# Kernel optimization log

Hardware: AMD Instinct MI355X
Metric: run time of the kernel (lower is better)

The kernel has to match this reference:

```python
import jax, jax.numpy as jnp
import numpy as np
import math

B, S, H, NH = 4, 1024, 1024, 16
HD = H // NH  # 64
MAX_REL = 127


def relative_position_encoding(depth, max_length, max_relative_position):
    vocab_size = max_relative_position * 2 + 1
    range_vec = np.arange(max_length)
    distance = range_vec[None, :] - range_vec[:, None]  # matches range_mat - range_mat.T
    final_mat = np.clip(distance, -max_relative_position, max_relative_position) + max_relative_position
    position = np.arange(vocab_size, dtype=np.float32)[:, None]
    div_term = np.exp(np.arange(0, depth, 2, dtype=np.float32) * (-math.log(10000.0) / depth))
    table = np.zeros((vocab_size, depth), dtype=np.float32)
    table[:, 0::2] = np.sin(position * div_term)
    table[:, 1::2] = np.cos(position * div_term)
    return jnp.asarray(table[final_mat])  # [max_length, max_length, depth]


def setup_inputs() -> dict:
    key = jax.random.key(0)
    ks = jax.random.split(key, 4)
    sc = 0.02
    return {
        "hidden_states": jax.random.normal(ks[0], (B, S, H), dtype=jnp.float32),
        "Wq": jax.random.normal(ks[1], (H, H), dtype=jnp.float32) * sc,
        "bq": jnp.zeros((H,), dtype=jnp.float32),
        "Wk": jax.random.normal(ks[2], (H, H), dtype=jnp.float32) * sc,
        "bk": jnp.zeros((H,), dtype=jnp.float32),
        "Wv": jax.random.normal(ks[3], (H, H), dtype=jnp.float32) * sc,
        "bv": jnp.zeros((H,), dtype=jnp.float32),
        "rel_pos": relative_position_encoding(HD, S, MAX_REL),  # [S, S, HD] sinusoidal buffer
    }


def reference(hidden_states, Wq, bq, Wk, bk, Wv, bv, rel_pos):
    b, s, h = hidden_states.shape

    def heads(x):  # [b,s,h] -> [b,nh,s,hd]
        return x.reshape(b, s, NH, HD).transpose(0, 2, 1, 3)

    q = heads(hidden_states @ Wq.T + bq)
    k = heads(hidden_states @ Wk.T + bk)
    v = heads(hidden_states @ Wv.T + bv)

    scores = jnp.einsum("bhqd,bhkd->bhqk", q, k)
    # query-relative-key positional term
    scores = scores + jnp.einsum("bhqd,qkd->bhqk", q, rel_pos)
    scores = scores / math.sqrt(HD)

    probs = jax.nn.softmax(scores, axis=-1)  # dropout p=0 (eval)

    ctx = jnp.einsum("bhqk,bhkd->bhqd", probs, v)
    # prob-relative-value positional term
    ctx = ctx + jnp.einsum("bhqk,qkd->bhqd", probs, rel_pos)

    return ctx.transpose(0, 2, 1, 3).reshape(b, s, h)
```

## Files before the change

### kernel.cpp

```cpp
#include <hip/hip_runtime.h>
#include <stdint.h>


typedef __bf16 bf16x8 __attribute__((ext_vector_type(8)));
typedef float f32x4 __attribute__((ext_vector_type(4)));
typedef uint16_t u16x8 __attribute__((ext_vector_type(8)));
typedef uint16_t u16x4 __attribute__((ext_vector_type(4)));

#define K2E 0.18033688011112042f

__device__ __forceinline__ float hw_exp2(float x) {
    return __builtin_amdgcn_exp2f(x);
}
__device__ __forceinline__ uint16_t f2bf(float f) {
    uint32_t u = __builtin_bit_cast(uint32_t, f);
    return (uint16_t)((u + 0x7FFFu + ((u >> 16) & 1u)) >> 16);
}
__device__ __forceinline__ uint16_t f2bf_rn(float f) {
    return __builtin_bit_cast(uint16_t, (__bf16)f);
}
__device__ __forceinline__ float bf2f(uint16_t h) {
    uint32_t u = ((uint32_t)h) << 16;
    return __builtin_bit_cast(float, u);
}
__device__ __forceinline__ f32x4 mfma16(bf16x8 a, bf16x8 b, f32x4 c) {
    return __builtin_amdgcn_mfma_f32_16x16x32_bf16(a, b, c, 0, 0, 0);
}
__device__ __forceinline__ bf16x8 ldg8(const uint16_t* p) {
    return __builtin_bit_cast(bf16x8, *(const u16x8*)p);
}
__device__ __forceinline__ bf16x8 lds8(const void* base, int byteoff) {
    return __builtin_bit_cast(bf16x8, *(const u16x8*)((const char*)base + byteoff));
}

__global__ void k_cast_all(const float* __restrict__ hs, const float* __restrict__ wq,
                           const float* __restrict__ wk, const float* __restrict__ wv,
                           const float* __restrict__ rel,
                           uint16_t* __restrict__ hs_bf, uint16_t* __restrict__ w_bf,
                           uint16_t* __restrict__ tab, uint16_t* __restrict__ tabT) {
    int b = blockIdx.x;
    if (b >= 3584) {
        int idx = (b - 3584) * 256 + threadIdx.x;
        int j = idx >> 6, d = idx & 63;
        float v = 0.0f;
        if (j < 255) v = rel[((size_t)512 * 1024 + (512 + j - 127)) * 64 + d];
        uint16_t h = f2bf(v);
        tab[j * 64 + d] = h;
        tabT[d * 256 + j] = h;
        return;
    }
    const float* src;
    uint16_t* dst;
    int i;
    if (b < 2048)      { src = hs; dst = hs_bf;           i = b * 256 + threadIdx.x; }
    else if (b < 2560) { src = wq; dst = w_bf;            i = (b - 2048) * 256 + threadIdx.x; }
    else if (b < 3072) { src = wk; dst = w_bf + 1048576;  i = (b - 2560) * 256 + threadIdx.x; }
    else               { src = wv; dst = w_bf + 2097152;  i = (b - 3072) * 256 + threadIdx.x; }
    float4 a = ((const float4*)src)[2 * i];
    float4 c = ((const float4*)src)[2 * i + 1];
    u16x8 o;
    o[0] = f2bf(a.x); o[1] = f2bf(a.y); o[2] = f2bf(a.z); o[3] = f2bf(a.w);
    o[4] = f2bf(c.x); o[5] = f2bf(c.y); o[6] = f2bf(c.z); o[7] = f2bf(c.w);
    ((u16x8*)dst)[i] = o;
}

__launch_bounds__(256)
__global__ void k_gemm_qkv3(const uint16_t* __restrict__ A, const uint16_t* __restrict__ Wt,
                            const float* __restrict__ bq, const float* __restrict__ bk,
                            const float* __restrict__ bvp, uint16_t* __restrict__ qout,
                            uint16_t* __restrict__ kout, uint16_t* __restrict__ vt) {
    __shared__ uint16_t As[128 * 64];
    __shared__ uint16_t Bs[128 * 64];
    int bid = blockIdx.x;
    int xcd = bid & 7, idx = bid >> 3;
    int m0 = (xcd * 4 + (idx & 3)) * 128;
    int n0 = (idx >> 2) * 128;
    int tid = threadIdx.x;
    int w = tid >> 6, l = tid & 63, lg = l >> 4, ln = l & 15;
    int wm = w >> 1, wn = w & 1;
    int lrow = tid >> 3, lcol = (tid & 7) * 8;
    f32x4 acc[4][4] = {};
    for (int kt = 0; kt < 16; ++kt) {
        int k0 = kt * 64;
        __syncthreads();
#pragma unroll
        for (int c = 0; c < 4; ++c) {
            int row = c * 32 + lrow;
            __builtin_amdgcn_global_load_lds(
                (const __attribute__((address_space(1))) void*)(A + (size_t)(m0 + row) * 1024 + k0 + lcol),
                (__attribute__((address_space(3))) void*)&As[row * 64 + lcol], 16, 0, 0);
            __builtin_amdgcn_global_load_lds(
                (const __attribute__((address_space(1))) void*)(Wt + (size_t)(n0 + row) * 1024 + k0 + lcol),
                (__attribute__((address_space(3))) void*)&Bs[row * 64 + lcol], 16, 0, 0);
        }
        __syncthreads();
#pragma unroll
        for (int ks = 0; ks < 2; ++ks) {
            bf16x8 af[4], bfr[4];
#pragma unroll
            for (int mi = 0; mi < 4; ++mi)
                af[mi] = ldg8(&As[(wm * 64 + mi * 16 + ln) * 64 + ks * 32 + lg * 8]);
#pragma unroll
            for (int ni = 0; ni < 4; ++ni)
                bfr[ni] = ldg8(&Bs[(wn * 64 + ni * 16 + ln) * 64 + ks * 32 + lg * 8]);
#pragma unroll
            for (int mi = 0; mi < 4; ++mi)
#pragma unroll
                for (int ni = 0; ni < 4; ++ni)
                    acc[mi][ni] = mfma16(af[mi], bfr[ni], acc[mi][ni]);
        }
    }
    int b = m0 >> 10, srow = (m0 & 1023) + wm * 64;
#pragma unroll
    for (int ni = 0; ni < 4; ++ni) {
        int n = n0 + wn * 64 + ni * 16 + ln;
        int which = n >> 10, nr = n & 1023;
        const float* bp = which == 0 ? bq : (which == 1 ? bk : bvp);
        float bb = bp[nr];
        int h = nr >> 6, d = nr & 63;
        if (which < 2) {
            uint16_t* base = which == 0 ? qout : kout;
#pragma unroll
            for (int mi = 0; mi < 4; ++mi)
#pragma unroll
                for (int r = 0; r < 4; ++r) {
                    int s = srow + mi * 16 + lg * 4 + r;
                    base[(((size_t)(b * 16 + h)) * 1024 + s) * 64 + d] = f2bf(acc[mi][ni][r] + bb);
                }
        } else {
#pragma unroll
            for (int mi = 0; mi < 4; ++mi) {
                int s0 = srow + mi * 16 + lg * 4;
                u16x4 pv;
#pragma unroll
                for (int r = 0; r < 4; ++r) pv[r] = f2bf(acc[mi][ni][r] + bb);
                *(u16x4*)&vt[(((size_t)(b * 16 + h)) * 64 + d) * 1024 + s0] = pv;
            }
        }
    }
}

__launch_bounds__(256)
__global__ void k_r_gemm(const uint16_t* __restrict__ q, const uint16_t* __restrict__ tab,
                         uint16_t* __restrict__ R) {
    __shared__ uint16_t Qs[64 * 72];
    int m0 = blockIdx.x * 64;
    int tid = threadIdx.x;
    int w = tid >> 6, l = tid & 63, lg = l >> 4, ln = l & 15;
#pragma unroll
    for (int c = 0; c < 2; ++c) {
        int idx = c * 256 + tid; int row = idx >> 3, seg = idx & 7;
        *(u16x8*)&Qs[row * 72 + seg * 8] =
            *(const u16x8*)(q + (size_t)(m0 + row) * 64 + seg * 8);
    }
    __syncthreads();
    bf16x8 aq[4][2];
#pragma unroll
    for (int mi = 0; mi < 4; ++mi)
#pragma unroll
        for (int ks = 0; ks < 2; ++ks)
            aq[mi][ks] = ldg8(&Qs[(mi * 16 + ln) * 72 + ks * 32 + lg * 8]);
    f32x4 acc[4][4] = {};
#pragma unroll
    for (int ni = 0; ni < 4; ++ni) {
        int j = w * 64 + ni * 16 + ln;
#pragma unroll
        for (int ks = 0; ks < 2; ++ks) {
            bf16x8 bt = ldg8(tab + j * 64 + ks * 32 + lg * 8);
#pragma unroll
            for (int mi = 0; mi < 4; ++mi)
                acc[mi][ni] = mfma16(aq[mi][ks], bt, acc[mi][ni]);
        }
    }
#pragma unroll
    for (int ni = 0; ni < 4; ++ni)
#pragma unroll
        for (int mi = 0; mi < 4; ++mi)
#pragma unroll
            for (int r = 0; r < 4; ++r)
                R[(size_t)(m0 + mi * 16 + lg * 4 + r) * 256 + w * 64 + ni * 16 + ln] =
                    f2bf(acc[mi][ni][r]);
}

__device__ __forceinline__ void softmax_grp(
    const f32x4 (&acc)[4], int kt, int qbase, int ln, const uint16_t* __restrict__ Rrow,
    float rel_lo2, float rel_hi2, uint16_t* prow, int lg,
    float& lloc, float& slo, float& shi, uint32_t (&pk)[4][2]) {
    int cls = (kt * 64 - (qbase + 15) >= 127) ? 2
            : ((kt * 64 + 63 - qbase <= -127) ? 0 : 1);
    int qg = qbase + ln;
    float sv[16];
    if (cls == 2) {
#pragma unroll
        for (int m = 0; m < 4; ++m)
#pragma unroll
            for (int r = 0; r < 4; ++r) sv[m * 4 + r] = fmaf(acc[m][r], K2E, rel_hi2);
    } else if (cls == 0) {
#pragma unroll
        for (int m = 0; m < 4; ++m)
#pragma unroll
            for (int r = 0; r < 4; ++r) sv[m * 4 + r] = fmaf(acc[m][r], K2E, rel_lo2);
    } else {
#pragma unroll
        for (int m = 0; m < 4; ++m) {
            int base = kt * 64 + (m >> 1) * 32 + lg * 8 + (m & 1) * 4 - qg;
#pragma unroll
            for (int r = 0; r < 4; ++r) {
                int dj = base + r;
                int djc = dj < -127 ? -127 : (dj > 127 ? 127 : dj);
                float rel = bf2f(Rrow[djc + 127]);
                sv[m * 4 + r] = (acc[m][r] + rel) * K2E;
            }
        }
    }
    float pm[4];
    if (cls == 1) {
#pragma unroll
        for (int m = 0; m < 4; ++m) {
            int base = kt * 64 + (m >> 1) * 32 + lg * 8 + (m & 1) * 4 - qg;
            uint32_t w0 = 0, w1 = 0;
            float ps = 0.f;
#pragma unroll
            for (int r = 0; r < 4; ++r) {
                float P = hw_exp2(sv[m * 4 + r]);
                ps += P;
                uint32_t h = f2bf_rn(P);
                int dj = base + r;
                if (dj <= -127) slo += P;
                else if (dj >= 127) shi += P;
                else prow[dj + 127] = (uint16_t)h;
                if (r < 2) w0 |= h << (16 * r); else w1 |= h << (16 * (r - 2));
            }
            pm[m] = ps;
            pk[m][0] = w0; pk[m][1] = w1;
        }
    } else {
#pragma unroll
        for (int m = 0; m < 4; ++m) {
            uint32_t w0 = 0, w1 = 0;
            float ps = 0.f;
#pragma unroll
            for (int r = 0; r < 4; ++r) {
                float P = hw_exp2(sv[m * 4 + r]);
                ps += P;
                uint32_t h = f2bf_rn(P);
                if (r < 2) w0 |= h << (16 * r); else w1 |= h << (16 * (r - 2));
            }
            pm[m] = ps;
            pk[m][0] = w0; pk[m][1] = w1;
        }
        float ts = (pm[0] + pm[1]) + (pm[2] + pm[3]);
        if (cls == 2) shi += ts; else slo += ts;
    }
    lloc += (pm[0] + pm[1]) + (pm[2] + pm[3]);
}

__launch_bounds__(256, 2)
__global__ void k_attn_fused(const uint16_t* __restrict__ qb, const uint16_t* __restrict__ kb,
                             const uint16_t* __restrict__ vtb, const uint16_t* __restrict__ Rb,
                             const uint16_t* __restrict__ tabT, float* __restrict__ out) {
    __shared__ uint16_t Pagg[128 * 256];
    __shared__ uint16_t Kb[64 * 64];
    __shared__ uint16_t Vb[64 * 64];
    int bid = blockIdx.x;
    bid = (bid & 7) * 64 + (bid >> 3);
    int bh = bid >> 3, q0 = (bid & 7) * 128;
    int tid = threadIdx.x;
    int w = tid >> 6, l = tid & 63, lg = l >> 4, ln = l & 15;
    int qbaseA = q0 + w * 16, qbaseB = qbaseA + 64;
    int qA = qbaseA + ln, qB = qA + 64;
    bf16x8 qfA[2], qfB[2];
    {
        const uint16_t* qr = qb + ((size_t)bh * 1024 + qA) * 64;
        qfA[0] = ldg8(qr + lg * 8); qfA[1] = ldg8(qr + 32 + lg * 8);
        qr += 64 * 64;
        qfB[0] = ldg8(qr + lg * 8); qfB[1] = ldg8(qr + 32 + lg * 8);
    }
    const uint16_t* RrowA = Rb + ((size_t)bh * 1024 + qA) * 256;
    const uint16_t* RrowB = RrowA + 64 * 256;
    uint16_t* prowA = &Pagg[(w * 16 + ln) * 256];
    uint16_t* prowB = &Pagg[(64 + w * 16 + ln) * 256];
    {
        u16x8* pa = (u16x8*)&Pagg[(w * 16) * 256];
        u16x8* pb2 = (u16x8*)&Pagg[(64 + w * 16) * 256];
#pragma unroll
        for (int i = 0; i < 8; ++i) { pa[i * 64 + l] = (u16x8)0; pb2[i * 64 + l] = (u16x8)0; }
    }
    float relA_lo = bf2f(RrowA[0]) * K2E, relA_hi = bf2f(RrowA[254]) * K2E;
    float relB_lo = bf2f(RrowB[0]) * K2E, relB_hi = bf2f(RrowB[254]) * K2E;
    const int r0 = tid >> 3, c16 = tid & 7;
    const int r1 = 32 + r0;
    const int slotK0 = (r0 & 3) | ((r0 >> 1) & 4), slotK1 = (r1 & 3) | ((r1 >> 1) & 4);
    const int waK0 = (r0 * 128 + c16 * 16) ^ (slotK0 << 4);
    const int waK1 = (r1 * 128 + c16 * 16) ^ (slotK1 << 4);
    const int waV0 = (r0 * 128 + c16 * 16) ^ ((r0 & 7) << 4);
    const int waV1 = (r1 * 128 + c16 * 16) ^ ((r1 & 7) << 4);
    const uint16_t* kt_base = kb + ((size_t)bh * 1024) * 64;
    const uint16_t* vt_base = vtb + (size_t)bh * 64 * 1024;
    u16x8 kc0 = *(const u16x8*)(kt_base + (size_t)r0 * 64 + c16 * 8);
    u16x8 kc1 = *(const u16x8*)(kt_base + (size_t)r1 * 64 + c16 * 8);
    u16x8 vc0 = *(const u16x8*)(vt_base + (size_t)r0 * 1024 + c16 * 8);
    u16x8 vc1 = *(const u16x8*)(vt_base + (size_t)r1 * 1024 + c16 * 8);
    float llocA = 0.f, sloA = 0.f, shiA = 0.f;
    float llocB = 0.f, sloB = 0.f, shiB = 0.f;
    f32x4 oaccA[4] = {}, oaccB[4] = {};
    for (int kt = 0; kt < 16; ++kt) {
        __syncthreads();
        *(u16x8*)((char*)Kb + waK0) = kc0;
        *(u16x8*)((char*)Kb + waK1) = kc1;
        *(u16x8*)((char*)Vb + waV0) = vc0;
        *(u16x8*)((char*)Vb + waV1) = vc1;
        __syncthreads();
        if (kt < 15) {
            const uint16_t* kn = kt_base + (size_t)(kt + 1) * 64 * 64;
            const uint16_t* vn = vt_base + (kt + 1) * 64;
            kc0 = *(const u16x8*)(kn + (size_t)r0 * 64 + c16 * 8);
            kc1 = *(const u16x8*)(kn + (size_t)r1 * 64 + c16 * 8);
            vc0 = *(const u16x8*)(vn + (size_t)r0 * 1024 + c16 * 8);
            vc1 = *(const u16x8*)(vn + (size_t)r1 * 1024 + c16 * 8);
        }
        f32x4 accA[4] = {}, accB[4] = {};
#pragma unroll
        for (int m = 0; m < 4; ++m) {
            int rowp = ((m >> 1) << 5) + ((ln >> 2) << 3) + ((m & 1) << 2) + (ln & 3);
            bf16x8 a0 = lds8(Kb, (rowp * 128 + lg * 16) ^ ((ln & 7) << 4));
            bf16x8 a1 = lds8(Kb, (rowp * 128 + 64 + lg * 16) ^ ((ln & 7) << 4));
            accA[m] = mfma16(a0, qfA[0], accA[m]);
            accA[m] = mfma16(a1, qfA[1], accA[m]);
            accB[m] = mfma16(a0, qfB[0], accB[m]);
            accB[m] = mfma16(a1, qfB[1], accB[m]);
        }
        uint32_t pkA[4][2], pkB[4][2];
        softmax_grp(accA, kt, qbaseA, ln, RrowA, relA_lo, relA_hi, prowA, lg,
                    llocA, sloA, shiA, pkA);
        softmax_grp(accB, kt, qbaseB, ln, RrowB, relB_lo, relB_hi, prowB, lg,
                    llocB, sloB, shiB, pkB);
#pragma unroll
        for (int ks = 0; ks < 2; ++ks) {
            uint32_t fa[4] = {pkA[2 * ks][0], pkA[2 * ks][1], pkA[2 * ks + 1][0], pkA[2 * ks + 1][1]};
            uint32_t fb[4] = {pkB[2 * ks][0], pkB[2 * ks][1], pkB[2 * ks + 1][0], pkB[2 * ks + 1][1]};
            bf16x8 apA = __builtin_bit_cast(bf16x8, fa);
            bf16x8 apB = __builtin_bit_cast(bf16x8, fb);
#pragma unroll
            for (int nt = 0; nt < 4; ++nt) {
                int row = nt * 16 + ln;
                bf16x8 bv = lds8(Vb, (row * 128 + (ks * 4 + lg) * 16) ^ ((ln & 7) << 4));
                oaccA[nt] = mfma16(apA, bv, oaccA[nt]);
                oaccB[nt] = mfma16(apB, bv, oaccB[nt]);
            }
        }
    }
    llocA += __shfl_xor(llocA, 16); llocA += __shfl_xor(llocA, 32);
    sloA  += __shfl_xor(sloA, 16);  sloA  += __shfl_xor(sloA, 32);
    shiA  += __shfl_xor(shiA, 16);  shiA  += __shfl_xor(shiA, 32);
    llocB += __shfl_xor(llocB, 16); llocB += __shfl_xor(llocB, 32);
    sloB  += __shfl_xor(sloB, 16);  sloB  += __shfl_xor(sloB, 32);
    shiB  += __shfl_xor(shiB, 16);  shiB  += __shfl_xor(shiB, 32);
    if (lg == 0) {
        prowA[0] = f2bf(sloA); prowA[254] = f2bf(shiA);
        prowB[0] = f2bf(sloB); prowB[254] = f2bf(shiB);
    }
#pragma unroll
    for (int ks8 = 0; ks8 < 8; ++ks8) {
        bf16x8 apA = ldg8(&Pagg[(w * 16 + ln) * 256 + ks8 * 32 + lg * 8]);
        bf16x8 apB = ldg8(&Pagg[(64 + w * 16 + ln) * 256 + ks8 * 32 + lg * 8]);
#pragma unroll
        for (int nt = 0; nt < 4; ++nt) {
            bf16x8 bt = ldg8(tabT + (size_t)(nt * 16 + ln) * 256 + ks8 * 32 + lg * 8);
            oaccA[nt] = mfma16(apA, bt, oaccA[nt]);
            oaccB[nt] = mfma16(apB, bt, oaccB[nt]);
        }
    }
    float rinvA[4], rinvB[4];
#pragma unroll
    for (int r = 0; r < 4; ++r) {
        rinvA[r] = 1.0f / __shfl(llocA, lg * 4 + r);
        rinvB[r] = 1.0f / __shfl(llocB, lg * 4 + r);
    }
    int b = bh >> 4, h = bh & 15;
#pragma unroll
    for (int nt = 0; nt < 4; ++nt) {
#pragma unroll
        for (int r = 0; r < 4; ++r) {
            int qoA = q0 + w * 16 + lg * 4 + r;
            out[((size_t)b * 1024 + qoA) * 1024 + h * 64 + nt * 16 + ln] = oaccA[nt][r] * rinvA[r];
            out[((size_t)b * 1024 + qoA + 64) * 1024 + h * 64 + nt * 16 + ln] = oaccB[nt][r] * rinvB[r];
        }
    }
}

extern "C" void kernel_launch(void* const* d_in, const int* in_sizes, int n_in,
                              void* d_out, int out_size, void* d_ws, size_t ws_size,
                              hipStream_t stream) {
    const float* hs  = (const float*)d_in[0];
    const float* Wq  = (const float*)d_in[1];
    const float* bq  = (const float*)d_in[2];
    const float* Wk  = (const float*)d_in[3];
    const float* bk  = (const float*)d_in[4];
    const float* Wv  = (const float*)d_in[5];
    const float* bv  = (const float*)d_in[6];
    const float* rel = (const float*)d_in[7];
    float* out = (float*)d_out;
    char* ws = (char*)d_ws;

    uint16_t* hs_bf = (uint16_t*)(ws);
    uint16_t* W_bf  = (uint16_t*)(ws + 8388608);
    uint16_t* q_bf  = (uint16_t*)(ws + 14680064);
    uint16_t* k_bf  = (uint16_t*)(ws + 23068672);
    uint16_t* vt_bf = (uint16_t*)(ws + 31457280);
    uint16_t* R_bf  = (uint16_t*)(ws + 48234496);
    uint16_t* tab   = (uint16_t*)(ws + 81788928);
    uint16_t* tabT  = (uint16_t*)(ws + 81821696);

    k_cast_all<<<3648, 256, 0, stream>>>(hs, Wq, Wk, Wv, rel, hs_bf, W_bf, tab, tabT);

    k_gemm_qkv3<<<768, 256, 0, stream>>>(hs_bf, W_bf, bq, bk, bv, q_bf, k_bf, vt_bf);
    k_r_gemm<<<1024, 256, 0, stream>>>(q_bf, tab, R_bf);

    k_attn_fused<<<512, 256, 0, stream>>>(q_bf, k_bf, vt_bf, R_bf, tabT, out);
}
```

Before: 132.4 us.

## Stage QKV GEMM epilogue through swizzled LDS for coalesced stores; add setprio

The QKV projection epilogue now writes bias-added bf16 results into a swizzled shared-memory tile and then issues 16-byte coalesced global stores, for both the head-major Q/K layout and the transposed V layout. Before, each lane wrote scattered 2-byte or 8-byte elements. Separately, the attention loop raises wave priority around the MFMA sections with s_setprio so matrix work is favoured over softmax in other waves. The cost is extra LDS traffic and barriers in the epilogue.

```diff
diff --git a/kernel.cpp b/kernel.cpp
--- a/kernel.cpp
+++ b/kernel.cpp
@@ -69,8 +69,9 @@
                             const float* __restrict__ bq, const float* __restrict__ bk,
                             const float* __restrict__ bvp, uint16_t* __restrict__ qout,
                             uint16_t* __restrict__ kout, uint16_t* __restrict__ vt) {
-    __shared__ uint16_t As[128 * 64];
-    __shared__ uint16_t Bs[128 * 64];
+    __shared__ uint16_t Sh[2 * 128 * 64];
+    uint16_t* As = Sh;
+    uint16_t* Bs = Sh + 8192;
     int bid = blockIdx.x;
     int xcd = bid & 7, idx = bid >> 3;
     int m0 = (xcd * 4 + (idx & 3)) * 128;
@@ -110,32 +111,60 @@
                     acc[mi][ni] = mfma16(af[mi], bfr[ni], acc[mi][ni]);
         }
     }
-    int b = m0 >> 10, srow = (m0 & 1023) + wm * 64;
-#pragma unroll
-    for (int ni = 0; ni < 4; ++ni) {
-        int n = n0 + wn * 64 + ni * 16 + ln;
-        int which = n >> 10, nr = n & 1023;
-        const float* bp = which == 0 ? bq : (which == 1 ? bk : bvp);
-        float bb = bp[nr];
-        int h = nr >> 6, d = nr & 63;
-        if (which < 2) {
-            uint16_t* base = which == 0 ? qout : kout;
+    int b = m0 >> 10, s0r = m0 & 1023;
+    int which = n0 >> 10, nbase = n0 & 1023;
+    __syncthreads();
+    if (which < 2) {
+        uint16_t* qk = which == 0 ? qout : kout;
+        const float* bp = which == 0 ? bq : bk;
+#pragma unroll
+        for (int ni = 0; ni < 4; ++ni) {
+            int d2 = wn * 64 + ni * 16 + ln;
+            float bb = bp[nbase + d2];
 #pragma unroll
             for (int mi = 0; mi < 4; ++mi)
 #pragma unroll
                 for (int r = 0; r < 4; ++r) {
-                    int s = srow + mi * 16 + lg * 4 + r;
-                    base[(((size_t)(b * 16 + h)) * 1024 + s) * 64 + d] = f2bf(acc[mi][ni][r] + bb);
+                    int s2 = wm * 64 + mi * 16 + lg * 4 + r;
+                    *(uint16_t*)((char*)Sh + ((s2 * 256 + d2 * 2) ^ (((s2 >> 2) & 7) << 4))) =
+                        f2bf(acc[mi][ni][r] + bb);
                 }
-        } else {
+        }
+        __syncthreads();
+#pragma unroll
+        for (int hh = 0; hh < 2; ++hh) {
+            int h = (nbase >> 6) + hh;
+#pragma unroll
+            for (int i = 0; i < 4; ++i) {
+                int s2 = i * 32 + w * 8 + (l >> 3);
+                int d2 = hh * 64 + (l & 7) * 8;
+                u16x8 vv = *(u16x8*)((char*)Sh + ((s2 * 256 + d2 * 2) ^ (((s2 >> 2) & 7) << 4)));
+                *(u16x8*)&qk[(((size_t)(b * 16 + h)) * 1024 + s0r + s2) * 64 + (d2 & 63)] = vv;
+            }
+        }
+    } else {
+#pragma unroll
+        for (int ni = 0; ni < 4; ++ni) {
+            int d2 = wn * 64 + ni * 16 + ln;
+            float bb = bvp[nbase + d2];
 #pragma unroll
             for (int mi = 0; mi < 4; ++mi) {
-                int s0 = srow + mi * 16 + lg * 4;
+                int s2 = wm * 64 + mi * 16 + lg * 4;
                 u16x4 pv;
 #pragma unroll
                 for (int r = 0; r < 4; ++r) pv[r] = f2bf(acc[mi][ni][r] + bb);
-                *(u16x4*)&vt[(((size_t)(b * 16 + h)) * 64 + d) * 1024 + s0] = pv;
-            }
+                *(u16x4*)((char*)Sh + ((d2 * 256 + s2 * 2) ^ ((d2 & 7) << 4))) = pv;
+            }
+        }
+        __syncthreads();
+#pragma unroll
+        for (int i = 0; i < 8; ++i) {
+            int d2 = i * 16 + w * 4 + (l >> 4);
+            int s2 = (l & 15) * 8;
+            u16x8 vv = *(u16x8*)((char*)Sh + ((d2 * 256 + s2 * 2) ^ ((d2 & 7) << 4)));
+            int nr = nbase + d2;
+            int h = nr >> 6, d = nr & 63;
+            *(u16x8*)&vt[(((size_t)(b * 16 + h)) * 64 + d) * 1024 + s0r + s2] = vv;
         }
     }
 }
@@ -320,6 +349,7 @@
             vc1 = *(const u16x8*)(vn + (size_t)r1 * 1024 + c16 * 8);
         }
         f32x4 accA[4] = {}, accB[4] = {};
+        __builtin_amdgcn_s_setprio(1);
 #pragma unroll
         for (int m = 0; m < 4; ++m) {
             int rowp = ((m >> 1) << 5) + ((ln >> 2) << 3) + ((m & 1) << 2) + (ln & 3);
@@ -330,11 +360,13 @@
             accB[m] = mfma16(a0, qfB[0], accB[m]);
             accB[m] = mfma16(a1, qfB[1], accB[m]);
         }
+        __builtin_amdgcn_s_setprio(0);
         uint32_t pkA[4][2], pkB[4][2];
         softmax_grp(accA, kt, qbaseA, ln, RrowA, relA_lo, relA_hi, prowA, lg,
                     llocA, sloA, shiA, pkA);
         softmax_grp(accB, kt, qbaseB, ln, RrowB, relB_lo, relB_hi, prowB, lg,
                     llocB, sloB, shiB, pkB);
+        __builtin_amdgcn_s_setprio(1);
 #pragma unroll
         for (int ks = 0; ks < 2; ++ks) {
             uint32_t fa[4] = {pkA[2 * ks][0], pkA[2 * ks][1], pkA[2 * ks + 1][0], pkA[2 * ks + 1][1]};
@@ -349,6 +381,7 @@
                 oaccB[nt] = mfma16(apB, bv, oaccB[nt]);
             }
         }
+        __builtin_amdgcn_s_setprio(0);
     }
     llocA += __shfl_xor(llocA, 16); llocA += __shfl_xor(llocA, 32);
     sloA  += __shfl_xor(sloA, 16);  sloA  += __shfl_xor(sloA, 32);
```

Result: faster. 129.0 us (-2.6%).
